# Kernel tuning notes

Hardware: AMD Instinct MI355X
Metric: run time of the kernel (lower is better)

The kernel has to match this reference:

```python
import jax, jax.numpy as jnp
import numpy as np
from jax import lax

B, C_IN, H, W = 16, 2048, 16, 16
HIDDEN, N_ANC = 512, 9
N_POS, N_NEG = 2048, 2048
TOT = B * N_ANC * H * W  # 36864 = flat conf logits; also rows of reg.view(-1,4)


def _xyxy_to_cxcywh(b):
    x1, y1, x2, y2 = b[..., 0], b[..., 1], b[..., 2], b[..., 3]
    return jnp.stack([(x1 + x2) * 0.5, (y1 + y2) * 0.5, x2 - x1, y2 - y1], axis=-1)


def _cxcywh_to_xyxy(b):
    cx, cy, w, h = b[..., 0], b[..., 1], b[..., 2], b[..., 3]
    return jnp.stack([cx - w * 0.5, cy - h * 0.5, cx + w * 0.5, cy + h * 0.5], axis=-1)


def _rand_boxes(key, n):
    # valid xyxy boxes on the 16x16 feature-map coordinate grid, w,h in [1,4]
    k1, k2 = jax.random.split(key)
    xy = jax.random.uniform(k1, (n, 2), jnp.float32) * 12.0
    wh = 1.0 + jax.random.uniform(k2, (n, 2), jnp.float32) * 3.0
    return jnp.concatenate([xy, xy + wh], axis=-1)


def setup_inputs() -> dict:
    key = jax.random.key(0)
    ks = jax.random.split(key, 10)
    feature_map = jax.random.normal(ks[0], (B, C_IN, H, W), jnp.float32)
    pos_anc_ind = jax.random.randint(ks[1], (N_POS,), 0, TOT)
    neg_anc_ind = jax.random.randint(ks[2], (N_NEG,), 0, TOT)
    pos_anc_coords = _rand_boxes(ks[3], N_POS)
    gt_bboxes_pos = _rand_boxes(ks[4], N_POS)
    s1 = 1.0 / np.sqrt(C_IN * 9)
    W1 = jax.random.uniform(ks[5], (HIDDEN, C_IN, 3, 3), jnp.float32, -s1, s1)
    b1 = jnp.zeros((HIDDEN,), jnp.float32)
    s2 = 1.0 / np.sqrt(HIDDEN)
    Wc = jax.random.uniform(ks[6], (N_ANC, HIDDEN), jnp.float32, -s2, s2)
    bc = jnp.zeros((N_ANC,), jnp.float32)
    Wr = jax.random.uniform(ks[7], (N_ANC * 4, HIDDEN), jnp.float32, -s2, s2)
    br = jnp.zeros((N_ANC * 4,), jnp.float32)
    return {"feature_map": feature_map, "pos_anc_coords": pos_anc_coords,
            "gt_bboxes_pos": gt_bboxes_pos, "W1": W1, "b1": b1, "Wc": Wc,
            "bc": bc, "Wr": Wr, "br": br,
            "pos_anc_ind": pos_anc_ind, "neg_anc_ind": neg_anc_ind}


def generate_proposals(anchors, offsets):
    a = _xyxy_to_cxcywh(anchors)
    p = jnp.stack([a[:, 0] + offsets[:, 0] * a[:, 2],
                   a[:, 1] + offsets[:, 1] * a[:, 3],
                   a[:, 2] * jnp.exp(offsets[:, 2]),
                   a[:, 3] * jnp.exp(offsets[:, 3])], axis=-1)
    return _cxcywh_to_xyxy(p)


def calc_gt_offsets(anc, gt):
    a = _xyxy_to_cxcywh(anc)
    g = _xyxy_to_cxcywh(gt)
    tx = (g[:, 0] - a[:, 0]) / a[:, 2]
    ty = (g[:, 1] - a[:, 1]) / a[:, 3]
    tw = jnp.log(g[:, 2] / a[:, 2])
    th = jnp.log(g[:, 3] / a[:, 3])
    return jnp.stack([tx, ty, tw, th], axis=-1)


def reference(feature_map, pos_anc_coords, gt_bboxes_pos, W1, b1, Wc, bc, Wr, br,
              pos_anc_ind, neg_anc_ind):
    # ProposalModule: conv3x3 -> (dropout=identity in eval) -> relu -> 1x1 heads
    out = lax.conv_general_dilated(feature_map, W1, (1, 1), 'SAME',
                                   dimension_numbers=('NCHW', 'OIHW', 'NCHW'))
    out = jax.nn.relu(out + b1[None, :, None, None])
    conf = jnp.einsum('bchw,oc->bohw', out, Wc) + bc[None, :, None, None]   # [B,9,H,W]
    reg = jnp.einsum('bchw,oc->bohw', out, Wr) + br[None, :, None, None]    # [B,36,H,W]
    # irregular flat gathers, exactly mirroring torch .flatten()/.view(-1,4)
    conf_pos = conf.reshape(-1)[pos_anc_ind]
    conf_neg = conf.reshape(-1)[neg_anc_ind]
    offsets_pos = reg.reshape(-1, 4)[pos_anc_ind]
    proposals = generate_proposals(pos_anc_coords, offsets_pos)
    gt_offsets = calc_gt_offsets(pos_anc_coords, gt_bboxes_pos)
    # BCE-with-logits, targets 1 for pos / 0 for neg, reduction='sum' / B
    cls_loss = (jnp.sum(jax.nn.softplus(-conf_pos)) + jnp.sum(jax.nn.softplus(conf_neg))) / B
    # smooth L1 (beta=1), reduction='sum' / B
    d = offsets_pos - gt_offsets
    ad = jnp.abs(d)
    reg_loss = jnp.sum(jnp.where(ad < 1.0, 0.5 * d * d, ad - 0.5)) / B
    total_rpn_loss = 1.0 * cls_loss + 5.0 * reg_loss  # w_conf=1, w_reg=5
    return total_rpn_loss, proposals
```

## Files before the change

kernel.cpp:

```cpp
#include <hip/hip_runtime.h>
#include <hip/hip_bf16.h>
#include <stdint.h>

#define CIN 2048
#define HID 512
#define NPOS 2048
#define NNEG 2048

#define BM 256
#define BN 128
#define BK 64
#define NSPLIT 4
#define A_ELEMS (BM * BK)
#define B_ELEMS (BN * BK)

typedef __attribute__((ext_vector_type(8))) short s16x8;
typedef __attribute__((ext_vector_type(4))) short s16x4;
typedef __attribute__((ext_vector_type(4))) float f32x4;
typedef unsigned short ushort_t;

static __device__ __forceinline__ unsigned short f2bf(float f) {
    union { float f; unsigned int i; } v; v.f = f;
    unsigned int r = v.i + 0x7FFF + ((v.i >> 16) & 1);
    return (unsigned short)(r >> 16);
}

typedef __attribute__((address_space(1))) const void gvoid_t;
typedef __attribute__((address_space(3))) void lvoid_t;
static __device__ __forceinline__ void gload16(const void* g, void* l) {
    __builtin_amdgcn_global_load_lds((gvoid_t*)g, (lvoid_t*)l, 16, 0, 0);
}

__global__ __launch_bounds__(256) void k_prep(const float* __restrict__ F,
                                              const float* __restrict__ W1,
                                              ushort_t* __restrict__ Fp,
                                              ushort_t* __restrict__ Wt2) {
    __shared__ float tile[64][17];
    __shared__ float buf[512 * 9];
    int bid = blockIdx.x;
    int t = threadIdx.x;
    if (bid < 256) {
        int b = bid >> 4, y = bid & 15;
        for (int ic0 = 0; ic0 < CIN; ic0 += 64) {
            {
                int ci = t >> 2, xg = t & 3;
                const float4 v = *(const float4*)&F[((size_t)(b * CIN + ic0 + ci) * 16 + y) * 16 + xg * 4];
                tile[ci][xg * 4 + 0] = v.x;
                tile[ci][xg * 4 + 1] = v.y;
                tile[ci][xg * 4 + 2] = v.z;
                tile[ci][xg * 4 + 3] = v.w;
            }
            __syncthreads();
            {
                int x = t >> 4, cig = t & 15;
                s16x4 o;
#pragma unroll
                for (int j = 0; j < 4; ++j) o[j] = (short)f2bf(tile[cig * 4 + j][x]);
                *(s16x4*)&Fp[((size_t)(b * 18 + y + 1) * 18 + (x + 1)) * CIN + ic0 + cig * 4] = o;
            }
            __syncthreads();
        }
    } else if (bid < 768) {
        int oc = bid - 256;
        for (int ic0 = 0; ic0 < CIN; ic0 += 512) {
            const float* src = W1 + ((size_t)oc * CIN + ic0) * 9;
            for (int i = t; i < 512 * 9; i += 256) buf[i] = src[i];
            __syncthreads();
            for (int s = t; s < 9 * 64; s += 256) {
                int k = s >> 6, g = s & 63;
                s16x8 v;
#pragma unroll
                for (int j = 0; j < 8; ++j) v[j] = (short)f2bf(buf[(g * 8 + j) * 9 + k]);
                *(s16x8*)&Wt2[((size_t)(k * HID + oc)) * CIN + ic0 + g * 8] = v;
            }
            __syncthreads();
        }
    } else {
        const s16x8 z = {0, 0, 0, 0, 0, 0, 0, 0};
        for (int idx = (bid - 768) * 256 + t; idx < 16 * 68 * 256; idx += 64 * 256) {
            int seg = idx & 255;
            int cell = (idx >> 8) % 68;
            int b = idx / (68 * 256);
            int Y, X;
            if (cell < 18)      { Y = 0;         X = cell; }
            else if (cell < 36) { Y = 17;        X = cell - 18; }
            else if (cell < 52) { Y = cell - 35; X = 0; }
            else                { Y = cell - 51; X = 17; }
            *(s16x8*)&Fp[((size_t)(b * 18 + Y) * 18 + X) * CIN + seg * 8] = z;
        }
    }
}

__global__ __launch_bounds__(512, 2) void k_gemm(const ushort_t* __restrict__ Fp,
                                                 const ushort_t* __restrict__ Wt2,
                                                 float* __restrict__ Part) {
    extern __shared__ ushort_t ldsbuf[];
    ushort_t* As = ldsbuf;
    ushort_t* Bs = ldsbuf + 3 * A_ELEMS;

    int bid = blockIdx.x;
    int pair = bid & 15, rb = bid >> 4;
    int split = pair >> 2, cb = pair & 3;
    int icBase = split * (CIN / NSPLIT);
    int m0 = rb * BM, oc0 = cb * BN;
    int t = threadIdx.x;
    int wid = t >> 6, lane = t & 63;
    int wr = wid >> 1, wn = wid & 1;
    int hi = lane >> 4, lo = lane & 15;

    f32x4 acc[4][4];
#pragma unroll
    for (int a = 0; a < 4; ++a)
#pragma unroll
        for (int b = 0; b < 4; ++b) acc[a][b] = (f32x4){0.f, 0.f, 0.f, 0.f};

    int Abase[4], Bbase[2];
#pragma unroll
    for (int j = 0; j < 4; ++j) {
        int li = j * 512 + t;
        int row = li >> 3;
        int sg = (li & 7) ^ (row & 7);
        int m = m0 + row;
        int b = m >> 8, y = (m >> 4) & 15, x = m & 15;
        Abase[j] = ((b * 18 + y) * 18 + x) * CIN + sg * 8;
    }
#pragma unroll
    for (int j = 0; j < 2; ++j) {
        int li = j * 512 + t;
        int row = li >> 3;
        int sg = (li & 7) ^ (row & 7);
        Bbase[j] = (oc0 + row) * CIN + sg * 8;
    }
    int aidx[4][2], bidx[4][2];
#pragma unroll
    for (int fm = 0; fm < 4; ++fm)
#pragma unroll
        for (int ks = 0; ks < 2; ++ks) {
            int r = wr * 64 + fm * 16 + lo;
            aidx[fm][ks] = r * BK + ((ks * 32 + hi * 8) ^ ((r & 7) << 3));
            int rB = wn * 64 + fm * 16 + lo;
            bidx[fm][ks] = rB * BK + ((ks * 32 + hi * 8) ^ ((rB & 7) << 3));
        }

    const int nsteps = (CIN / NSPLIT / BK) * 9;

#define STAGE_A(BUF, S)                                                              \
    do {                                                                             \
        int kidx_ = (S) % 9, icc_ = (S) / 9;                                         \
        int ak_ = ((kidx_ / 3) * 18 + (kidx_ - 3 * (kidx_ / 3))) * CIN + icBase + icc_ * BK; \
        ushort_t* dA_ = As + (BUF) * A_ELEMS;                                        \
        _Pragma("unroll") for (int j_ = 0; j_ < 4; ++j_)                             \
            gload16(Fp + Abase[j_] + ak_, dA_ + (size_t)(j_ * 512 + t) * 8);         \
    } while (0)
#define STAGE_B(BUF, S)                                                              \
    do {                                                                             \
        int kidx_ = (S) % 9, icc_ = (S) / 9;                                         \
        int bk_ = kidx_ * HID * CIN + icBase + icc_ * BK;                            \
        ushort_t* dB_ = Bs + (BUF) * B_ELEMS;                                        \
        _Pragma("unroll") for (int j_ = 0; j_ < 2; ++j_)                             \
            gload16(Wt2 + Bbase[j_] + bk_, dB_ + (size_t)(j_ * 512 + t) * 8);        \
    } while (0)

    STAGE_A(0, 0); STAGE_B(0, 0);
    STAGE_A(1, 1); STAGE_B(1, 1);
    asm volatile("s_waitcnt vmcnt(6)" ::: "memory");
    __builtin_amdgcn_s_barrier();
    __builtin_amdgcn_sched_barrier(0);

    int bi = 0;
#pragma unroll 1
    for (int step = 0; step < nsteps; ++step) {
        const ushort_t* cA = As + bi * A_ELEMS;
        const ushort_t* cB = Bs + bi * B_ELEMS;
        int b2 = (bi >= 1) ? bi - 1 : 2;
        s16x8 af[4][2], bf0[2][2];
#pragma unroll
        for (int ks = 0; ks < 2; ++ks) {
#pragma unroll
            for (int fm = 0; fm < 4; ++fm) af[fm][ks] = *(const s16x8*)&cA[aidx[fm][ks]];
#pragma unroll
            for (int fn = 0; fn < 2; ++fn) bf0[fn][ks] = *(const s16x8*)&cB[bidx[fn][ks]];
        }
        if (step + 2 < nsteps) STAGE_A(b2, step + 2);
        asm volatile("s_waitcnt lgkmcnt(0)" ::: "memory");
        __builtin_amdgcn_sched_barrier(0);
        __builtin_amdgcn_s_setprio(1);
#pragma unroll
        for (int fm = 0; fm < 4; ++fm)
#pragma unroll
            for (int fn = 0; fn < 2; ++fn)
#pragma unroll
                for (int ks = 0; ks < 2; ++ks)
                    acc[fm][fn] = __builtin_amdgcn_mfma_f32_16x16x32_bf16(
                        af[fm][ks], bf0[fn][ks], acc[fm][fn], 0, 0, 0);
        __builtin_amdgcn_s_setprio(0);
        s16x8 bf1[2][2];
#pragma unroll
        for (int ks = 0; ks < 2; ++ks)
#pragma unroll
            for (int fn = 0; fn < 2; ++fn) bf1[fn][ks] = *(const s16x8*)&cB[bidx[2 + fn][ks]];
        if (step + 2 < nsteps) STAGE_B(b2, step + 2);
        asm volatile("s_waitcnt lgkmcnt(0)" ::: "memory");
        __builtin_amdgcn_sched_barrier(0);
        __builtin_amdgcn_s_setprio(1);
#pragma unroll
        for (int fm = 0; fm < 4; ++fm)
#pragma unroll
            for (int fn = 0; fn < 2; ++fn)
#pragma unroll
                for (int ks = 0; ks < 2; ++ks)
                    acc[fm][2 + fn] = __builtin_amdgcn_mfma_f32_16x16x32_bf16(
                        af[fm][ks], bf1[fn][ks], acc[fm][2 + fn], 0, 0, 0);
        __builtin_amdgcn_s_setprio(0);
        if (step + 2 < nsteps) {
            asm volatile("s_waitcnt vmcnt(6)" ::: "memory");
            __builtin_amdgcn_s_barrier();
            __builtin_amdgcn_sched_barrier(0);
        } else if (step + 1 < nsteps) {
            asm volatile("s_waitcnt vmcnt(0)" ::: "memory");
            __builtin_amdgcn_s_barrier();
            __builtin_amdgcn_sched_barrier(0);
        }
        bi = (bi == 2) ? 0 : bi + 1;
    }
#undef STAGE_A
#undef STAGE_B

#pragma unroll
    for (int fm = 0; fm < 4; ++fm)
#pragma unroll
        for (int fn = 0; fn < 4; ++fn)
#pragma unroll
            for (int r = 0; r < 4; ++r) {
                int gm = m0 + wr * 64 + fm * 16 + hi * 4 + r;
                int gn = oc0 + wn * 64 + fn * 16 + lo;
                Part[((size_t)split * 4096 + gm) * HID + gn] = acc[fm][fn][r];
            }
}

__global__ __launch_bounds__(256) void k_heads(const float* __restrict__ Part,
                                               const float* __restrict__ b1,
                                               const float* __restrict__ Wc,
                                               const float* __restrict__ bc,
                                               const float* __restrict__ Wr,
                                               const float* __restrict__ br,
                                               float* __restrict__ conf,
                                               float* __restrict__ reg) {
    __shared__ __align__(16) ushort_t Ah[64 * 64];
    __shared__ __align__(16) ushort_t Wh[48 * 64];
    int t = threadIdx.x;
    int wid = t >> 6, lane = t & 63;
    int hi = lane >> 4, lo = lane & 15;
    int row0 = blockIdx.x * 64;

    f32x4 acc[3];
#pragma unroll
    for (int fn = 0; fn < 3; ++fn) acc[fn] = (f32x4){0.f, 0.f, 0.f, 0.f};

#pragma unroll 1
    for (int kc = 0; kc < HID / 64; ++kc) {
        int k0 = kc * 64;
#pragma unroll
        for (int g = 0; g < 4; ++g) {
            int fid = g * 256 + t;
            int r = fid >> 4, c4 = (fid & 15) * 4;
            float4 s = {0.f, 0.f, 0.f, 0.f};
#pragma unroll
            for (int sp = 0; sp < NSPLIT; ++sp) {
                const float4 v = *(const float4*)&Part[((size_t)sp * 4096 + row0 + r) * HID + k0 + c4];
                s.x += v.x; s.y += v.y; s.z += v.z; s.w += v.w;
            }
            s.x = fmaxf(s.x + b1[k0 + c4 + 0], 0.f);
            s.y = fmaxf(s.y + b1[k0 + c4 + 1], 0.f);
            s.z = fmaxf(s.z + b1[k0 + c4 + 2], 0.f);
            s.w = fmaxf(s.w + b1[k0 + c4 + 3], 0.f);
            s16x4 o = {(short)f2bf(s.x), (short)f2bf(s.y), (short)f2bf(s.z), (short)f2bf(s.w)};
            int phys = r * 64 + ((((c4 >> 3) ^ (r & 7)) << 3) | (c4 & 7));
            *(s16x4*)&Ah[phys] = o;
        }
#pragma unroll
        for (int i = 0; i < 2; ++i) {
            int sid = i * 256 + t;
            if (sid < 384) {
                int o = sid >> 3, sg = sid & 7;
                s16x8 v;
#pragma unroll
                for (int j = 0; j < 8; ++j) {
                    float w = 0.f;
                    if (o < 9) w = Wc[o * HID + k0 + sg * 8 + j];
                    else if (o < 45) w = Wr[(size_t)(o - 9) * HID + k0 + sg * 8 + j];
                    v[j] = (short)f2bf(w);
                }
                *(s16x8*)&Wh[o * 64 + ((sg ^ (o & 7)) << 3)] = v;
            }
        }
        __syncthreads();
        int rA = wid * 16 + lo;
        s16x8 a_[2];
#pragma unroll
        for (int ks = 0; ks < 2; ++ks)
            a_[ks] = *(const s16x8*)&Ah[rA * 64 + ((ks * 32 + hi * 8) ^ ((rA & 7) << 3))];
#pragma unroll
        for (int fn = 0; fn < 3; ++fn) {
            int rB = fn * 16 + lo;
#pragma unroll
            for (int ks = 0; ks < 2; ++ks) {
                s16x8 b_ = *(const s16x8*)&Wh[rB * 64 + ((ks * 32 + hi * 8) ^ ((rB & 7) << 3))];
                acc[fn] = __builtin_amdgcn_mfma_f32_16x16x32_bf16(a_[ks], b_, acc[fn], 0, 0, 0);
            }
        }
        __syncthreads();
    }
#pragma unroll
    for (int fn = 0; fn < 3; ++fn)
#pragma unroll
        for (int r = 0; r < 4; ++r) {
            int gm = row0 + wid * 16 + hi * 4 + r;
            int o = fn * 16 + lo;
            float v = acc[fn][r];
            if (o < 9) conf[gm * 9 + o] = v + bc[o];
            else if (o < 45) reg[gm * 36 + (o - 9)] = v + br[o - 9];
        }
}

static __device__ __forceinline__ float softplus(float x) {
    return log1pf(expf(-fabsf(x))) + fmaxf(x, 0.f);
}

__global__ __launch_bounds__(256) void k_loss(const float* __restrict__ conf,
                                              const float* __restrict__ reg,
                                              const int* __restrict__ pos_ind,
                                              const int* __restrict__ neg_ind,
                                              const float* __restrict__ anc,
                                              const float* __restrict__ gt,
                                              float* __restrict__ out) {
    int t = threadIdx.x;
    float cls = 0.f, rloss = 0.f;
    for (int p = t; p < NPOS; p += 256) {
        int ind = pos_ind[p];
        {
            int b = ind / 2304, r = ind % 2304;
            int c = r >> 8, r2 = r & 255;
            float cv = conf[(b * 256 + r2) * 9 + c];
            cls += softplus(-cv);
        }
        float off[4];
#pragma unroll
        for (int j = 0; j < 4; ++j) {
            int e = 4 * ind + j;
            int b = e / 9216, r = e % 9216;
            int c = r >> 8, r2 = r & 255;
            off[j] = reg[(b * 256 + r2) * 36 + c];
        }
        float ax1 = anc[4 * p], ay1 = anc[4 * p + 1], ax2 = anc[4 * p + 2], ay2 = anc[4 * p + 3];
        float acx = (ax1 + ax2) * 0.5f, acy = (ay1 + ay2) * 0.5f;
        float aw = ax2 - ax1, ah = ay2 - ay1;
        float pcx = acx + off[0] * aw, pcy = acy + off[1] * ah;
        float pw = aw * expf(off[2]), ph = ah * expf(off[3]);
        out[1 + 4 * p + 0] = pcx - pw * 0.5f;
        out[1 + 4 * p + 1] = pcy - ph * 0.5f;
        out[1 + 4 * p + 2] = pcx + pw * 0.5f;
        out[1 + 4 * p + 3] = pcy + ph * 0.5f;
        float gx1 = gt[4 * p], gy1 = gt[4 * p + 1], gx2 = gt[4 * p + 2], gy2 = gt[4 * p + 3];
        float gcx = (gx1 + gx2) * 0.5f, gcy = (gy1 + gy2) * 0.5f;
        float gw = gx2 - gx1, gh = gy2 - gy1;
        float tv[4];
        tv[0] = (gcx - acx) / aw;
        tv[1] = (gcy - acy) / ah;
        tv[2] = logf(gw / aw);
        tv[3] = logf(gh / ah);
#pragma unroll
        for (int j = 0; j < 4; ++j) {
            float d = off[j] - tv[j];
            float ad = fabsf(d);
            rloss += (ad < 1.f) ? 0.5f * d * d : ad - 0.5f;
        }
    }
    for (int q = t; q < NNEG; q += 256) {
        int ind = neg_ind[q];
        int b = ind / 2304, r = ind % 2304;
        int c = r >> 8, r2 = r & 255;
        float cv = conf[(b * 256 + r2) * 9 + c];
        cls += softplus(cv);
    }
    __shared__ float s1[256], s2[256];
    s1[t] = cls;
    s2[t] = rloss;
    __syncthreads();
    for (int s = 128; s > 0; s >>= 1) {
        if (t < s) {
            s1[t] += s1[t + s];
            s2[t] += s2[t + s];
        }
        __syncthreads();
    }
    if (t == 0) out[0] = (s1[0] + 5.f * s2[0]) / 16.f;
}

extern "C" void kernel_launch(void* const* d_in, const int* in_sizes, int n_in,
                              void* d_out, int out_size, void* d_ws, size_t ws_size,
                              hipStream_t stream) {
    const float* F   = (const float*)d_in[0];
    const float* anc = (const float*)d_in[1];
    const float* gt  = (const float*)d_in[2];
    const float* W1  = (const float*)d_in[3];
    const float* b1  = (const float*)d_in[4];
    const float* Wc  = (const float*)d_in[5];
    const float* bc  = (const float*)d_in[6];
    const float* Wr  = (const float*)d_in[7];
    const float* br  = (const float*)d_in[8];
    const int* pos_ind = (const int*)d_in[9];
    const int* neg_ind = (const int*)d_in[10];
    float* out = (float*)d_out;

    char* ws = (char*)d_ws;
    const size_t FP_BYTES   = (size_t)16 * 18 * 18 * CIN * 2;
    const size_t WT_BYTES   = (size_t)9 * HID * CIN * 2;
    const size_t PART_ONE   = (size_t)4096 * HID * 4;
    const size_t CONF_BYTES = (size_t)4096 * 9 * 4;

    ushort_t* Fp  = (ushort_t*)ws;
    ushort_t* Wt2 = (ushort_t*)(ws + FP_BYTES);
    float* Part   = (float*)(ws + FP_BYTES + WT_BYTES);
    float* conf   = (float*)(ws + FP_BYTES + WT_BYTES + (size_t)NSPLIT * PART_ONE);
    float* reg    = (float*)(ws + FP_BYTES + WT_BYTES + (size_t)NSPLIT * PART_ONE + CONF_BYTES);

    const int GEMM_LDS = 3 * (A_ELEMS + B_ELEMS) * 2;
    hipFuncSetAttribute((const void*)k_gemm, hipFuncAttributeMaxDynamicSharedMemorySize, GEMM_LDS);

    k_prep<<<832, 256, 0, stream>>>(F, W1, Fp, Wt2);
    k_gemm<<<(4096 / BM) * (HID / BN) * NSPLIT, 512, GEMM_LDS, stream>>>(Fp, Wt2, Part);
    k_heads<<<64, 256, 0, stream>>>(Part, b1, Wc, bc, Wr, br, conf, reg);
    k_loss<<<1, 256, 0, stream>>>(conf, reg, pos_ind, neg_ind, anc, gt, out);
}
```

Measured before the change: 147.1 us.

## Merge GEMM LDS phases, widen heads grid, and use 1024-thread loss block

The GEMM main loop now issues the next A and B global-to-LDS stages up front and does all fragment reads and MFMAs in one phase, removing the intermediate lgkmcnt waits and sched barriers. The heads kernel now handles 16 rows per block over 256 blocks. It stages the full 512-wide activation and weight rows into dynamic LDS once, and a single wave runs the MFMAs. The loss kernel uses 1024 threads instead of 256. Together these aim to cut wait/barrier overhead and raise parallelism in the small tail kernels, at the cost of redundant weight conversion per heads block and three idle waves during its MFMA phase.

```diff
diff --git a/kernel.cpp b/kernel.cpp
--- a/kernel.cpp
+++ b/kernel.cpp
@@ -173,44 +173,24 @@
         const ushort_t* cA = As + bi * A_ELEMS;
         const ushort_t* cB = Bs + bi * B_ELEMS;
         int b2 = (bi >= 1) ? bi - 1 : 2;
-        s16x8 af[4][2], bf0[2][2];
+        if (step + 2 < nsteps) { STAGE_A(b2, step + 2); STAGE_B(b2, step + 2); }
+        s16x8 af[4][2], bf[4][2];
 #pragma unroll
         for (int ks = 0; ks < 2; ++ks) {
 #pragma unroll
             for (int fm = 0; fm < 4; ++fm) af[fm][ks] = *(const s16x8*)&cA[aidx[fm][ks]];
 #pragma unroll
-            for (int fn = 0; fn < 2; ++fn) bf0[fn][ks] = *(const s16x8*)&cB[bidx[fn][ks]];
-        }
-        if (step + 2 < nsteps) STAGE_A(b2, step + 2);
-        asm volatile("s_waitcnt lgkmcnt(0)" ::: "memory");
-        __builtin_amdgcn_sched_barrier(0);
+            for (int fn = 0; fn < 4; ++fn) bf[fn][ks] = *(const s16x8*)&cB[bidx[fn][ks]];
+        }
         __builtin_amdgcn_s_setprio(1);
 #pragma unroll
         for (int fm = 0; fm < 4; ++fm)
 #pragma unroll
-            for (int fn = 0; fn < 2; ++fn)
+            for (int fn = 0; fn < 4; ++fn)
 #pragma unroll
                 for (int ks = 0; ks < 2; ++ks)
                     acc[fm][fn] = __builtin_amdgcn_mfma_f32_16x16x32_bf16(
-                        af[fm][ks], bf0[fn][ks], acc[fm][fn], 0, 0, 0);
-        __builtin_amdgcn_s_setprio(0);
-        s16x8 bf1[2][2];
-#pragma unroll
-        for (int ks = 0; ks < 2; ++ks)
-#pragma unroll
-            for (int fn = 0; fn < 2; ++fn) bf1[fn][ks] = *(const s16x8*)&cB[bidx[2 + fn][ks]];
-        if (step + 2 < nsteps) STAGE_B(b2, step + 2);
-        asm volatile("s_waitcnt lgkmcnt(0)" ::: "memory");
-        __builtin_amdgcn_sched_barrier(0);
-        __builtin_amdgcn_s_setprio(1);
-#pragma unroll
-        for (int fm = 0; fm < 4; ++fm)
-#pragma unroll
-            for (int fn = 0; fn < 2; ++fn)
-#pragma unroll
-                for (int ks = 0; ks < 2; ++ks)
-                    acc[fm][2 + fn] = __builtin_amdgcn_mfma_f32_16x16x32_bf16(
-                        af[fm][ks], bf1[fn][ks], acc[fm][2 + fn], 0, 0, 0);
+                        af[fm][ks], bf[fn][ks], acc[fm][fn], 0, 0, 0);
         __builtin_amdgcn_s_setprio(0);
         if (step + 2 < nsteps) {
             asm volatile("s_waitcnt vmcnt(6)" ::: "memory");
@@ -246,76 +226,68 @@
                                                const float* __restrict__ br,
                                                float* __restrict__ conf,
                                                float* __restrict__ reg) {
-    __shared__ __align__(16) ushort_t Ah[64 * 64];
-    __shared__ __align__(16) ushort_t Wh[48 * 64];
+    extern __shared__ ushort_t hsm[];
+    ushort_t* Ah = hsm;
+    ushort_t* Wh = hsm + 16 * HID;
     int t = threadIdx.x;
     int wid = t >> 6, lane = t & 63;
     int hi = lane >> 4, lo = lane & 15;
-    int row0 = blockIdx.x * 64;
+    int row0 = blockIdx.x * 16;
+
+#pragma unroll
+    for (int i = 0; i < 8; ++i) {
+        int pos = i * 256 + t;
+        int r = pos >> 7, c4 = (pos & 127) * 4;
+        float4 s = {0.f, 0.f, 0.f, 0.f};
+#pragma unroll
+        for (int sp = 0; sp < NSPLIT; ++sp) {
+            const float4 v = *(const float4*)&Part[((size_t)sp * 4096 + row0 + r) * HID + c4];
+            s.x += v.x; s.y += v.y; s.z += v.z; s.w += v.w;
+        }
+        s.x = fmaxf(s.x + b1[c4 + 0], 0.f);
+        s.y = fmaxf(s.y + b1[c4 + 1], 0.f);
+        s.z = fmaxf(s.z + b1[c4 + 2], 0.f);
+        s.w = fmaxf(s.w + b1[c4 + 3], 0.f);
+        s16x4 o = {(short)f2bf(s.x), (short)f2bf(s.y), (short)f2bf(s.z), (short)f2bf(s.w)};
+        int phys = r * HID + ((((c4 >> 3) ^ (r & 7)) << 3) | (c4 & 7));
+        *(s16x4*)&Ah[phys] = o;
+    }
+#pragma unroll
+    for (int i = 0; i < 12; ++i) {
+        int sid = i * 256 + t;
+        int o = sid >> 6, sg = sid & 63;
+        s16x8 v;
+#pragma unroll
+        for (int j = 0; j < 8; ++j) {
+            float w = 0.f;
+            if (o < 9) w = Wc[o * HID + sg * 8 + j];
+            else if (o < 45) w = Wr[(size_t)(o - 9) * HID + sg * 8 + j];
+            v[j] = (short)f2bf(w);
+        }
+        *(s16x8*)&Wh[o * HID + ((sg ^ (o & 7)) << 3)] = v;
+    }
+    __syncthreads();
+    if (wid != 0) return;
 
     f32x4 acc[3];
 #pragma unroll
     for (int fn = 0; fn < 3; ++fn) acc[fn] = (f32x4){0.f, 0.f, 0.f, 0.f};
-
 #pragma unroll 1
-    for (int kc = 0; kc < HID / 64; ++kc) {
-        int k0 = kc * 64;
-#pragma unroll
-        for (int g = 0; g < 4; ++g) {
-            int fid = g * 256 + t;
-            int r = fid >> 4, c4 = (fid & 15) * 4;
-            float4 s = {0.f, 0.f, 0.f, 0.f};
-#pragma unroll
-            for (int sp = 0; sp < NSPLIT; ++sp) {
-                const float4 v = *(const float4*)&Part[((size_t)sp * 4096 + row0 + r) * HID + k0 + c4];
-                s.x += v.x; s.y += v.y; s.z += v.z; s.w += v.w;
-            }
-            s.x = fmaxf(s.x + b1[k0 + c4 + 0], 0.f);
-            s.y = fmaxf(s.y + b1[k0 + c4 + 1], 0.f);
-            s.z = fmaxf(s.z + b1[k0 + c4 + 2], 0.f);
-            s.w = fmaxf(s.w + b1[k0 + c4 + 3], 0.f);
-            s16x4 o = {(short)f2bf(s.x), (short)f2bf(s.y), (short)f2bf(s.z), (short)f2bf(s.w)};
-            int phys = r * 64 + ((((c4 >> 3) ^ (r & 7)) << 3) | (c4 & 7));
-            *(s16x4*)&Ah[phys] = o;
-        }
-#pragma unroll
-        for (int i = 0; i < 2; ++i) {
-            int sid = i * 256 + t;
-            if (sid < 384) {
-                int o = sid >> 3, sg = sid & 7;
-                s16x8 v;
-#pragma unroll
-                for (int j = 0; j < 8; ++j) {
-                    float w = 0.f;
-                    if (o < 9) w = Wc[o * HID + k0 + sg * 8 + j];
-                    else if (o < 45) w = Wr[(size_t)(o - 9) * HID + k0 + sg * 8 + j];
-                    v[j] = (short)f2bf(w);
-                }
-                *(s16x8*)&Wh[o * 64 + ((sg ^ (o & 7)) << 3)] = v;
-            }
-        }
-        __syncthreads();
-        int rA = wid * 16 + lo;
-        s16x8 a_[2];
-#pragma unroll
-        for (int ks = 0; ks < 2; ++ks)
-            a_[ks] = *(const s16x8*)&Ah[rA * 64 + ((ks * 32 + hi * 8) ^ ((rA & 7) << 3))];
+    for (int kf = 0; kf < 16; ++kf) {
+        int rA = lo;
+        s16x8 a_ = *(const s16x8*)&Ah[rA * HID + ((kf * 32 + hi * 8) ^ ((rA & 7) << 3))];
 #pragma unroll
         for (int fn = 0; fn < 3; ++fn) {
             int rB = fn * 16 + lo;
-#pragma unroll
-            for (int ks = 0; ks < 2; ++ks) {
-                s16x8 b_ = *(const s16x8*)&Wh[rB * 64 + ((ks * 32 + hi * 8) ^ ((rB & 7) << 3))];
-                acc[fn] = __builtin_amdgcn_mfma_f32_16x16x32_bf16(a_[ks], b_, acc[fn], 0, 0, 0);
-            }
-        }
-        __syncthreads();
+            s16x8 b_ = *(const s16x8*)&Wh[rB * HID + ((kf * 32 + hi * 8) ^ ((rB & 7) << 3))];
+            acc[fn] = __builtin_amdgcn_mfma_f32_16x16x32_bf16(a_, b_, acc[fn], 0, 0, 0);
+        }
     }
 #pragma unroll
     for (int fn = 0; fn < 3; ++fn)
 #pragma unroll
         for (int r = 0; r < 4; ++r) {
-            int gm = row0 + wid * 16 + hi * 4 + r;
+            int gm = row0 + hi * 4 + r;
             int o = fn * 16 + lo;
             float v = acc[fn][r];
             if (o < 9) conf[gm * 9 + o] = v + bc[o];
@@ -327,16 +299,16 @@
     return log1pf(expf(-fabsf(x))) + fmaxf(x, 0.f);
 }
 
-__global__ __launch_bounds__(256) void k_loss(const float* __restrict__ conf,
-                                              const float* __restrict__ reg,
-                                              const int* __restrict__ pos_ind,
-                                              const int* __restrict__ neg_ind,
-                                              const float* __restrict__ anc,
-                                              const float* __restrict__ gt,
-                                              float* __restrict__ out) {
+__global__ __launch_bounds__(1024) void k_loss(const float* __restrict__ conf,
+                                               const float* __restrict__ reg,
+                                               const int* __restrict__ pos_ind,
+                                               const int* __restrict__ neg_ind,
+                                               const float* __restrict__ anc,
+                                               const float* __restrict__ gt,
+                                               float* __restrict__ out) {
     int t = threadIdx.x;
     float cls = 0.f, rloss = 0.f;
-    for (int p = t; p < NPOS; p += 256) {
+    for (int p = t; p < NPOS; p += 1024) {
         int ind = pos_ind[p];
         {
             int b = ind / 2304, r = ind % 2304;
@@ -376,18 +348,18 @@
             rloss += (ad < 1.f) ? 0.5f * d * d : ad - 0.5f;
         }
     }
-    for (int q = t; q < NNEG; q += 256) {
+    for (int q = t; q < NNEG; q += 1024) {
         int ind = neg_ind[q];
         int b = ind / 2304, r = ind % 2304;
         int c = r >> 8, r2 = r & 255;
         float cv = conf[(b * 256 + r2) * 9 + c];
         cls += softplus(cv);
     }
-    __shared__ float s1[256], s2[256];
+    __shared__ float s1[1024], s2[1024];
     s1[t] = cls;
     s2[t] = rloss;
     __syncthreads();
-    for (int s = 128; s > 0; s >>= 1) {
+    for (int s = 512; s > 0; s >>= 1) {
         if (t < s) {
             s1[t] += s1[t + s];
             s2[t] += s2[t + s];
@@ -427,9 +399,11 @@
 
     const int GEMM_LDS = 3 * (A_ELEMS + B_ELEMS) * 2;
     hipFuncSetAttribute((const void*)k_gemm, hipFuncAttributeMaxDynamicSharedMemorySize, GEMM_LDS);
+    const int HEADS_LDS = (16 + 48) * HID * 2;
+    hipFuncSetAttribute((const void*)k_heads, hipFuncAttributeMaxDynamicSharedMemorySize, HEADS_LDS);
 
     k_prep<<<832, 256, 0, stream>>>(F, W1, Fp, Wt2);
     k_gemm<<<(4096 / BM) * (HID / BN) * NSPLIT, 512, GEMM_LDS, stream>>>(Fp, Wt2, Part);
-    k_heads<<<64, 256, 0, stream>>>(Part, b1, Wc, bc, Wr, br, conf, reg);
-    k_loss<<<1, 256, 0, stream>>>(conf, reg, pos_ind, neg_ind, anc, gt, out);
-}
+    k_heads<<<256, 256, HEADS_LDS, stream>>>(Part, b1, Wc, bc, Wr, br, conf, reg);
+    k_loss<<<1, 1024, 0, stream>>>(conf, reg, pos_ind, neg_ind, anc, gt, out);
+}
```

After: 130.8 us. 11.1% less time.
